# Optimization experiments

Hardware: AMD Instinct MI355X
Metric: run time of the kernel (lower is better)

The kernel has to match this reference:

```python
import jax, jax.numpy as jnp
import numpy as np
import math

B, T, F, H, C = 512, 26, 2048, 1024, 22


def _lstm_cell(x_t, h, c, Wih, Whh, bih, bhh):
    # PyTorch gate order: i, f, g, o. Gates: [B, 4H]
    gates = x_t @ Wih.T + h @ Whh.T + bih + bhh
    i, f, g, o = jnp.split(gates, 4, axis=-1)
    c_new = jax.nn.sigmoid(f) * c + jax.nn.sigmoid(i) * jnp.tanh(g)
    h_new = jax.nn.sigmoid(o) * jnp.tanh(c_new)
    return h_new, c_new


def setup_inputs() -> dict:
    key = jax.random.key(0)
    ks = jax.random.split(key, 13)
    s_enc = 1.0 / math.sqrt(H)
    inp = {
        "x": jax.random.normal(ks[0], (B, T, F), jnp.float32),
        "enc_Wih": jax.random.normal(ks[1], (4 * H, F), jnp.float32) * s_enc,
        "enc_Whh": jax.random.normal(ks[2], (4 * H, H), jnp.float32) * s_enc,
        "enc_bih": jax.random.normal(ks[3], (4 * H,), jnp.float32) * s_enc,
        "enc_bhh": jax.random.normal(ks[4], (4 * H,), jnp.float32) * s_enc,
        "proj_W": jax.random.normal(ks[5], (H, H), jnp.float32) * s_enc,
        "proj_b": jax.random.normal(ks[6], (H,), jnp.float32) * s_enc,
        "dec_Wih": jax.random.normal(ks[7], (4 * H, H + F), jnp.float32) * s_enc,
        "dec_Whh": jax.random.normal(ks[8], (4 * H, H), jnp.float32) * s_enc,
        "dec_bih": jax.random.normal(ks[9], (4 * H,), jnp.float32) * s_enc,
        "dec_bhh": jax.random.normal(ks[10], (4 * H,), jnp.float32) * s_enc,
        "cls_W": jax.random.normal(ks[11], (C, H), jnp.float32) * s_enc,
        "cls_b": jax.random.normal(ks[12], (C,), jnp.float32) * s_enc,
    }
    return inp


def reference(x, enc_Wih, enc_Whh, enc_bih, enc_bhh, proj_W, proj_b,
              dec_Wih, dec_Whh, dec_bih, dec_bhh, cls_W, cls_b):
    # feature_extractor treated as identity (fusion_size == F)
    b, t, _ = x.shape
    h = x.shape[-1]  # noqa (F)

    # ---- Encoder LSTM over time (batch_first) ----
    def enc_step(carry, x_t):
        h_prev, c_prev = carry
        h_new, c_new = _lstm_cell(x_t, h_prev, c_prev, enc_Wih, enc_Whh, enc_bih, enc_bhh)
        return (h_new, c_new), h_new

    h0 = jnp.zeros((b, H), x.dtype)
    c0 = jnp.zeros((b, H), x.dtype)
    xs = jnp.swapaxes(x, 0, 1)  # [T, B, F]
    _, h_ts = jax.lax.scan(enc_step, (h0, c0), xs)  # [T, B, H]
    h_ts = jnp.swapaxes(h_ts, 0, 1)  # [B, T, H]

    proj_h_ts = h_ts @ proj_W.T + proj_b  # [B, T, H]
    inv_sqrt_h = 1.0 / math.sqrt(H)

    # ---- Decoder with per-step attention ----
    def dec_step(carry, x_t):
        dec_h, dec_c = carry
        # attention scores over encoder timesteps
        attn_logits = jnp.einsum('bh,bth->bt', dec_h, proj_h_ts) * inv_sqrt_h
        attn_w = jax.nn.softmax(attn_logits, axis=-1)
        attn = jnp.einsum('bt,bth->bh', attn_w, proj_h_ts)  # [B, H]
        inp_t = jnp.concatenate([x_t, attn], axis=1)  # [B, F+H]
        dec_h, dec_c = _lstm_cell(inp_t, dec_h, dec_c, dec_Wih, dec_Whh, dec_bih, dec_bhh)
        score = dec_h @ cls_W.T + cls_b  # [B, C]
        return (dec_h, dec_c), score

    _, scores = jax.lax.scan(dec_step, (h0, c0), xs)  # [T, B, C]
    return jnp.swapaxes(scores, 0, 1)  # [B, T, C]
```

## Files before the change

### kernel.cpp

```cpp
#include <hip/hip_runtime.h>

#define DB 512
#define DT 26
#define DF 2048
#define DH 1024
#define DG 4096
#define DC 22

typedef unsigned short u16;
typedef u16 u16x8 __attribute__((ext_vector_type(8)));
typedef __bf16 bf16x8 __attribute__((ext_vector_type(8)));
typedef float f32x4 __attribute__((ext_vector_type(4)));

#define MFMA(a, b, c) __builtin_amdgcn_mfma_f32_16x16x32_bf16((a), (b), (c), 0, 0, 0)

__device__ __forceinline__ float sigm(float x) { return 1.f / (1.f + __expf(-x)); }

__device__ __forceinline__ u16 f2b(float v) {
  unsigned u = __float_as_uint(v);
  return (u16)((u + 0x7FFFu + ((u >> 16) & 1u)) >> 16);
}
__device__ __forceinline__ float b2f(u16 h) {
  return __uint_as_float(((unsigned)h) << 16);
}
__device__ __forceinline__ void store_b4(u16* __restrict__ d, size_t o, float4 v) {
  ushort4 s;
  s.x = f2b(v.x); s.y = f2b(v.y); s.z = f2b(v.z); s.w = f2b(v.w);
  *(ushort4*)(d + o) = s;
}

template <int OUTBF>
__global__ __launch_bounds__(256) void gemm_bt(
    const u16* __restrict__ A1, long lda1, int K1,
    const u16* __restrict__ A2, long lda2,
    const u16* __restrict__ B, long ldb, const float* __restrict__ bias,
    void* __restrict__ Cp, long ldc, int M, int N, int K, int W)
{
  constexpr int LR = 72;
  __shared__ __align__(16) u16 sA[64 * LR];
  __shared__ __align__(16) u16 sB[128 * LR];
  const int tid = threadIdx.x, lane = tid & 63;
  const int wid = tid >> 6, wm = wid >> 1, wn = wid & 1;
  const int nbm = M >> 6;
  const int cpx = gridDim.x >> 3;
  const int swz = (blockIdx.x & 7) * cpx + (blockIdx.x >> 3);
  const int grpw = nbm * W;
  const int bn = (swz / grpw) * W + (swz % W);
  const int bm = (swz % grpw) / W;
  const size_t m0 = (size_t)bm << 6, n0 = (size_t)bn << 7;

  const int row = tid >> 3, c8 = tid & 7;
  u16x8 ra[2], rb[4];

  auto loadA = [&](int k0) {
    const u16* p; long lda; int kk;
    if (k0 < K1) { p = A1; lda = lda1; kk = k0; }
    else         { p = A2; lda = lda2; kk = k0 - K1; }
#pragma unroll
    for (int r = 0; r < 2; ++r)
      ra[r] = *(const u16x8*)(p + (m0 + row + r * 32) * (size_t)lda + (size_t)(kk + c8 * 8));
  };
  auto loadB = [&](int k0) {
#pragma unroll
    for (int r = 0; r < 4; ++r)
      rb[r] = *(const u16x8*)(B + (n0 + row + r * 32) * (size_t)ldb + (size_t)(k0 + c8 * 8));
  };
  loadA(0);
  loadB(0);

  f32x4 acc[2][4] = {};
  for (int k0 = 0; k0 < K; k0 += 64) {
    __syncthreads();
#pragma unroll
    for (int r = 0; r < 2; ++r) *(u16x8*)(sA + (row + r * 32) * LR + c8 * 8) = ra[r];
#pragma unroll
    for (int r = 0; r < 4; ++r) *(u16x8*)(sB + (row + r * 32) * LR + c8 * 8) = rb[r];
    __syncthreads();
    if (k0 + 64 < K) { loadA(k0 + 64); loadB(k0 + 64); }
#pragma unroll
    for (int ks = 0; ks < 2; ++ks) {
      const int ko = ks * 32 + (lane >> 4) * 8;
      bf16x8 af[2], bfr[4];
#pragma unroll
      for (int mi = 0; mi < 2; ++mi)
        af[mi] = *(const bf16x8*)(sA + ((wm << 5) + (mi << 4) + (lane & 15)) * LR + ko);
#pragma unroll
      for (int ni = 0; ni < 4; ++ni)
        bfr[ni] = *(const bf16x8*)(sB + ((wn << 6) + (ni << 4) + (lane & 15)) * LR + ko);
#pragma unroll
      for (int mi = 0; mi < 2; ++mi)
#pragma unroll
        for (int ni = 0; ni < 4; ++ni)
          acc[mi][ni] = MFMA(af[mi], bfr[ni], acc[mi][ni]);
    }
  }

#pragma unroll
  for (int mi = 0; mi < 2; ++mi) {
    const int row0 = (wm << 5) + (mi << 4) + ((lane >> 4) << 2);
#pragma unroll
    for (int ni = 0; ni < 4; ++ni) {
      const size_t gn = n0 + (size_t)((wn << 6) + (ni << 4) + (lane & 15));
      const float bv = bias[gn];
#pragma unroll
      for (int r = 0; r < 4; ++r) {
        const size_t gm = m0 + (size_t)(row0 + r);
        const float v = acc[mi][ni][r] + bv;
        if (OUTBF) ((u16*)Cp)[gm * (size_t)ldc + gn] = f2b(v);
        else       ((float*)Cp)[gm * (size_t)ldc + gn] = v;
      }
    }
  }
}

template <int DEC>
__global__ __launch_bounds__(512) void step_gemm(
    const u16* __restrict__ A, long lda, const u16* __restrict__ B, long ldb,
    const u16* __restrict__ xg, long ldxg, float* __restrict__ cst,
    u16* __restrict__ hout, int K, int first, int skipA)
{
  constexpr int LR = 72;
  __shared__ __align__(16) u16 sA[64 * LR];
  __shared__ __align__(16) u16 sB[128 * LR];
  const int tid = threadIdx.x, lane = tid & 63;
  const int wid = tid >> 6, wm = wid >> 1, wn = wid & 1;
  const int cpx = gridDim.x >> 3;
  const int swz = (blockIdx.x & 7) * cpx + (blockIdx.x >> 3);
  const int bn = swz >> 3, bm = swz & 7;
  const size_t m0 = (size_t)bm << 6, n0 = (size_t)bn << 7;

  const int row = tid >> 3, c8 = tid & 7;
  u16x8 ra, rb[2];
  auto loadA = [&](int k0) {
    ra = *(const u16x8*)(A + (m0 + row) * (size_t)lda + (size_t)(k0 + c8 * 8));
  };
  auto loadB = [&](int k0) {
#pragma unroll
    for (int r = 0; r < 2; ++r)
      rb[r] = *(const u16x8*)(B + (n0 + row + r * 64) * (size_t)ldb + (size_t)(k0 + c8 * 8));
  };

  f32x4 acc[4] = {};
  if (!skipA) {
    loadA(0);
    loadB(0);
    for (int k0 = 0; k0 < K; k0 += 64) {
      __syncthreads();
      *(u16x8*)(sA + row * LR + c8 * 8) = ra;
#pragma unroll
      for (int r = 0; r < 2; ++r) *(u16x8*)(sB + (row + r * 64) * LR + c8 * 8) = rb[r];
      __syncthreads();
      if (k0 + 64 < K) { loadA(k0 + 64); loadB(k0 + 64); }
#pragma unroll
      for (int ks = 0; ks < 2; ++ks) {
        const int ko = ks * 32 + (lane >> 4) * 8;
        bf16x8 af, bfr[4];
        af = *(const bf16x8*)(sA + ((wm << 4) + (lane & 15)) * LR + ko);
#pragma unroll
        for (int ni = 0; ni < 4; ++ni)
          bfr[ni] = *(const bf16x8*)(sB + ((wn << 6) + (ni << 4) + (lane & 15)) * LR + ko);
#pragma unroll
        for (int ni = 0; ni < 4; ++ni)
          acc[ni] = MFMA(af, bfr[ni], acc[ni]);
      }
    }
  }

  const int l = lane & 15;
  const int hg = (bn << 5) + (wn << 4) + l;
  const int row0 = (wm << 4) + ((lane >> 4) << 2);
#pragma unroll
  for (int r = 0; r < 4; ++r) {
    const int gm = (int)m0 + row0 + r;
    const u16* xr = xg + (size_t)gm * ldxg + n0 + (wn << 6) + l;
    const float gi = acc[0][r] + b2f(xr[0]);
    const float gf = acc[1][r] + b2f(xr[16]);
    const float gg = acc[2][r] + b2f(xr[32]);
    const float go = acc[3][r] + b2f(xr[48]);
    const size_t ch = ((size_t)gm << 10) + hg;
    const float cp = first ? 0.f : cst[ch];
    const float cn = sigm(gf) * cp + sigm(gi) * tanhf(gg);
    const float hn = sigm(go) * tanhf(cn);
    cst[ch] = cn;
    if (DEC) hout[((size_t)gm << 11) + 1024 + hg] = f2b(hn);
    else     hout[((size_t)gm << 10) + hg] = f2b(hn);
  }
}

__global__ __launch_bounds__(256) void cvt4_kernel(const float* __restrict__ src,
    u16* __restrict__ dst, int n4) {
  for (int i = blockIdx.x * 256 + threadIdx.x; i < n4; i += gridDim.x * 256) {
    float4 v = *(const float4*)(src + (size_t)i * 4);
    store_b4(dst, (size_t)i * 4, v);
  }
}

__global__ __launch_bounds__(256) void pack_perm_kernel(const float* __restrict__ src,
    long ld_src, long scol, int cols4, u16* __restrict__ dst, long ld_dst, long dcol) {
  const int total = DG * cols4;
  for (int i = blockIdx.x * 256 + threadIdx.x; i < total; i += gridDim.x * 256) {
    const int np = i / cols4, c4 = i - np * cols4;
    const int g = (np >> 4) & 3, h = ((np >> 6) << 4) | (np & 15);
    const int n = g * 1024 + h;
    float4 v = *(const float4*)(src + (size_t)n * ld_src + scol + (size_t)c4 * 4);
    store_b4(dst, (size_t)np * ld_dst + dcol + (size_t)c4 * 4, v);
  }
}

__global__ void pack_bias_perm_kernel(const float* __restrict__ a,
    const float* __restrict__ b, float* __restrict__ o) {
  int np = blockIdx.x * 256 + threadIdx.x;
  if (np < DG) {
    const int g = (np >> 4) & 3, h = ((np >> 6) << 4) | (np & 15);
    const int n = g * 1024 + h;
    o[np] = a[n] + b[n];
  }
}

template <int DO_ATTN>
__global__ __launch_bounds__(256) void attn_cls_kernel(
    const u16* __restrict__ projH, const u16* __restrict__ Zr, u16* __restrict__ Zw,
    const float* __restrict__ clsW, const float* __restrict__ clsb,
    float* __restrict__ out, int do_cls, int tprev)
{
  const int b = blockIdx.x, tid = threadIdx.x, lane = tid & 63, wid = tid >> 6;
  __shared__ float redc[DC][4];
  __shared__ float red[DT][4];
  __shared__ float wgt[DT];

  ushort4 hz = *(const ushort4*)(Zr + ((size_t)b << 11) + 1024 + tid * 4);
  float4 hv = make_float4(b2f(hz.x), b2f(hz.y), b2f(hz.z), b2f(hz.w));

  if (do_cls) {
    float acc[DC];
#pragma unroll
    for (int c = 0; c < DC; ++c) {
      const float4 w = *(const float4*)(clsW + ((size_t)c << 10) + tid * 4);
      acc[c] = hv.x * w.x + hv.y * w.y + hv.z * w.z + hv.w * w.w;
    }
#pragma unroll
    for (int c = 0; c < DC; ++c) {
      float v = acc[c];
#pragma unroll
      for (int off = 32; off; off >>= 1) v += __shfl_xor(v, off);
      if (lane == 0) redc[c][wid] = v;
    }
  }

  if (DO_ATTN) {
    float ph[DT][4];
    float p[DT];
#pragma unroll
    for (int t = 0; t < DT; ++t) {
      ushort4 pv = *(const ushort4*)(projH + (((size_t)t * DB + b) << 10) + tid * 4);
      ph[t][0] = b2f(pv.x); ph[t][1] = b2f(pv.y); ph[t][2] = b2f(pv.z); ph[t][3] = b2f(pv.w);
      p[t] = hv.x * ph[t][0] + hv.y * ph[t][1] + hv.z * ph[t][2] + hv.w * ph[t][3];
    }
#pragma unroll
    for (int t = 0; t < DT; ++t) {
#pragma unroll
      for (int off = 32; off; off >>= 1) p[t] += __shfl_xor(p[t], off);
      if (lane == 0) red[t][wid] = p[t];
    }
    __syncthreads();
    if (tid == 0) {
      float lg[DT];
      float mx = -1e30f;
#pragma unroll
      for (int t = 0; t < DT; ++t) {
        lg[t] = (red[t][0] + red[t][1] + red[t][2] + red[t][3]) * 0.03125f;
        mx = fmaxf(mx, lg[t]);
      }
      float s = 0.f;
#pragma unroll
      for (int t = 0; t < DT; ++t) { lg[t] = __expf(lg[t] - mx); s += lg[t]; }
      float inv = 1.f / s;
#pragma unroll
      for (int t = 0; t < DT; ++t) wgt[t] = lg[t] * inv;
    }
    __syncthreads();
    float4 a = make_float4(0, 0, 0, 0);
#pragma unroll
    for (int t = 0; t < DT; ++t) {
      const float w = wgt[t];
      a.x += w * ph[t][0]; a.y += w * ph[t][1]; a.z += w * ph[t][2]; a.w += w * ph[t][3];
    }
    store_b4(Zw, ((size_t)b << 11) + tid * 4, a);
  }

  if (do_cls) {
    __syncthreads();
    if (tid < DC)
      out[((size_t)b * DT + tprev) * DC + tid] =
          redc[tid][0] + redc[tid][1] + redc[tid][2] + redc[tid][3] + clsb[tid];
  }
}

extern "C" void kernel_launch(void* const* d_in, const int* in_sizes, int n_in,
                              void* d_out, int out_size, void* d_ws, size_t ws_size,
                              hipStream_t stream) {
  const float* x    = (const float*)d_in[0];
  const float* eWih = (const float*)d_in[1];
  const float* eWhh = (const float*)d_in[2];
  const float* ebih = (const float*)d_in[3];
  const float* ebhh = (const float*)d_in[4];
  const float* pW   = (const float*)d_in[5];
  const float* pb   = (const float*)d_in[6];
  const float* dWih = (const float*)d_in[7];
  const float* dWhh = (const float*)d_in[8];
  const float* dbih = (const float*)d_in[9];
  const float* dbhh = (const float*)d_in[10];
  const float* clsW = (const float*)d_in[11];
  const float* clsb = (const float*)d_in[12];
  float* out = (float*)d_out;

  char* p = (char*)d_ws;
  auto alloc = [&](size_t bytes) -> void* {
    char* r = p; p += (bytes + 255) & ~(size_t)255; return (void*)r;
  };
  u16* Xb    = (u16*)alloc((size_t)DB * DT * DF * 2);
  u16* eWx   = (u16*)alloc((size_t)DG * 2048 * 2);
  u16* eWh   = (u16*)alloc((size_t)DG * 1024 * 2);
  u16* dWx   = (u16*)alloc((size_t)DG * 2048 * 2);
  u16* dWah  = (u16*)alloc((size_t)DG * 2048 * 2);
  u16* pWb   = (u16*)alloc((size_t)DH * DH * 2);
  u16* Hb    = (u16*)alloc((size_t)DT * DB * DH * 2);
  u16* encXg = (u16*)alloc((size_t)DB * DT * DG * 2);
  u16* decXg = (u16*)alloc((size_t)DB * DT * DG * 2);
  u16* Z0    = (u16*)alloc((size_t)DB * 2048 * 2);
  u16* Z1    = (u16*)alloc((size_t)DB * 2048 * 2);
  float* eCs = (float*)alloc((size_t)DB * DH * 4);
  float* dCs = (float*)alloc((size_t)DB * DH * 4);
  float* ebs = (float*)alloc(DG * 4);
  float* dbs = (float*)alloc(DG * 4);
  u16* projHb = Xb;

  cvt4_kernel<<<2048, 256, 0, stream>>>(x, Xb, (int)((size_t)DB * DT * DF / 4));
  pack_perm_kernel<<<2048, 256, 0, stream>>>(eWih, DF, 0, DF / 4, eWx, 2048, 0);
  pack_perm_kernel<<<2048, 256, 0, stream>>>(eWhh, DH, 0, DH / 4, eWh, 1024, 0);
  pack_perm_kernel<<<2048, 256, 0, stream>>>(dWih, 3072, 0, DF / 4, dWx, 2048, 0);
  pack_perm_kernel<<<2048, 256, 0, stream>>>(dWih, 3072, 2048, DH / 4, dWah, 2048, 0);
  pack_perm_kernel<<<2048, 256, 0, stream>>>(dWhh, DH, 0, DH / 4, dWah, 2048, 1024);
  cvt4_kernel<<<1024, 256, 0, stream>>>(pW, pWb, DH * DH / 4);
  pack_bias_perm_kernel<<<16, 256, 0, stream>>>(ebih, ebhh, ebs);
  pack_bias_perm_kernel<<<16, 256, 0, stream>>>(dbih, dbhh, dbs);
  hipMemsetAsync(Z0, 0, (size_t)DB * 2048 * 2, stream);

  gemm_bt<1><<<6656, 256, 0, stream>>>(
      Xb, DF, DF, Xb, DF, eWx, DF, ebs, encXg, DG, DB * DT, DG, DF, 4);
  gemm_bt<1><<<6656, 256, 0, stream>>>(
      Xb, DF, DF, Xb, DF, dWx, DF, dbs, decXg, DG, DB * DT, DG, DF, 4);

  for (int t = 0; t < DT; ++t) {
    step_gemm<0><<<256, 512, 0, stream>>>(
        (t == 0) ? Hb : (Hb + (size_t)(t - 1) * DB * DH), DH, eWh, DH,
        encXg + (size_t)t * DG, (long)DT * DG, eCs,
        Hb + (size_t)t * DB * DH, 1024, t == 0, t == 0);
  }

  gemm_bt<1><<<1664, 256, 0, stream>>>(
      Hb, DH, DH, Hb, DH, pWb, DH, pb, projHb, DH, DT * DB, DH, DH, 1);

  for (int t = 0; t < DT; ++t) {
    u16* Zc = (t & 1) ? Z1 : Z0;
    u16* Zn = (t & 1) ? Z0 : Z1;
    attn_cls_kernel<1><<<DB, 256, 0, stream>>>(
        projHb, Zc, Zc, clsW, clsb, out, t > 0, t - 1);
    step_gemm<1><<<256, 512, 0, stream>>>(
        Zc, 2048, dWah, 2048, decXg + (size_t)t * DG, (long)DT * DG, dCs, Zn,
        (t == 0) ? 1024 : 2048, t == 0, 0);
  }
  attn_cls_kernel<0><<<DB, 256, 0, stream>>>(
      projHb, Z0, Z0, clsW, clsb, out, 1, DT - 1);
}
```

Before: 2.140 ms.

## Enlarge GEMM tile to 128x128 and load tiles directly into LDS

```diff
diff --git a/kernel.cpp b/kernel.cpp
--- a/kernel.cpp
+++ b/kernel.cpp
@@ -36,59 +36,50 @@
     const u16* __restrict__ B, long ldb, const float* __restrict__ bias,
     void* __restrict__ Cp, long ldc, int M, int N, int K, int W)
 {
-  constexpr int LR = 72;
-  __shared__ __align__(16) u16 sA[64 * LR];
-  __shared__ __align__(16) u16 sB[128 * LR];
-  const int tid = threadIdx.x, lane = tid & 63;
-  const int wid = tid >> 6, wm = wid >> 1, wn = wid & 1;
-  const int nbm = M >> 6;
+  __shared__ __align__(16) u16 sA[128 * 64];
+  __shared__ __align__(16) u16 sB[128 * 64];
+  const int tid = threadIdx.x, lane = tid & 63, wid = tid >> 6;
+  const int wm = wid >> 1, wn = wid & 1;
+  const int l15 = lane & 15, l4 = lane >> 4;
+  const int nbm = M >> 7;
   const int cpx = gridDim.x >> 3;
   const int swz = (blockIdx.x & 7) * cpx + (blockIdx.x >> 3);
   const int grpw = nbm * W;
   const int bn = (swz / grpw) * W + (swz % W);
   const int bm = (swz % grpw) / W;
-  const size_t m0 = (size_t)bm << 6, n0 = (size_t)bn << 7;
-
-  const int row = tid >> 3, c8 = tid & 7;
-  u16x8 ra[2], rb[4];
-
-  auto loadA = [&](int k0) {
-    const u16* p; long lda; int kk;
-    if (k0 < K1) { p = A1; lda = lda1; kk = k0; }
-    else         { p = A2; lda = lda2; kk = k0 - K1; }
-#pragma unroll
-    for (int r = 0; r < 2; ++r)
-      ra[r] = *(const u16x8*)(p + (m0 + row + r * 32) * (size_t)lda + (size_t)(kk + c8 * 8));
-  };
-  auto loadB = [&](int k0) {
-#pragma unroll
-    for (int r = 0; r < 4; ++r)
-      rb[r] = *(const u16x8*)(B + (n0 + row + r * 32) * (size_t)ldb + (size_t)(k0 + c8 * 8));
-  };
-  loadA(0);
-  loadB(0);
-
-  f32x4 acc[2][4] = {};
+  const size_t m0 = (size_t)bm << 7, n0 = (size_t)bn << 7;
+
+  f32x4 acc[4][4] = {};
   for (int k0 = 0; k0 < K; k0 += 64) {
-    __syncthreads();
-#pragma unroll
-    for (int r = 0; r < 2; ++r) *(u16x8*)(sA + (row + r * 32) * LR + c8 * 8) = ra[r];
-#pragma unroll
-    for (int r = 0; r < 4; ++r) *(u16x8*)(sB + (row + r * 32) * LR + c8 * 8) = rb[r];
-    __syncthreads();
-    if (k0 + 64 < K) { loadA(k0 + 64); loadB(k0 + 64); }
+    const u16* pA; long lda; int kk;
+    if (k0 < K1) { pA = A1; lda = lda1; kk = k0; }
+    else         { pA = A2; lda = lda2; kk = k0 - K1; }
+    __syncthreads();
+#pragma unroll
+    for (int g = 0; g < 4; ++g) {
+      const int cb = (wid * 4 + g) * 64;
+      const int chunk = cb + lane;
+      const int row = chunk >> 3, c8 = chunk & 7;
+      __builtin_amdgcn_global_load_lds(
+          (const __attribute__((address_space(1))) void*)(pA + (m0 + row) * (size_t)lda + kk + c8 * 8),
+          (__attribute__((address_space(3))) void*)((char*)sA + cb * 16), 16, 0, 0);
+      __builtin_amdgcn_global_load_lds(
+          (const __attribute__((address_space(1))) void*)(B + (n0 + row) * (size_t)ldb + k0 + c8 * 8),
+          (__attribute__((address_space(3))) void*)((char*)sB + cb * 16), 16, 0, 0);
+    }
+    __syncthreads();
 #pragma unroll
     for (int ks = 0; ks < 2; ++ks) {
-      const int ko = ks * 32 + (lane >> 4) * 8;
-      bf16x8 af[2], bfr[4];
-#pragma unroll
-      for (int mi = 0; mi < 2; ++mi)
-        af[mi] = *(const bf16x8*)(sA + ((wm << 5) + (mi << 4) + (lane & 15)) * LR + ko);
+      const int ko = ks * 32 + l4 * 8;
+      bf16x8 af[4], bfr[4];
+#pragma unroll
+      for (int mi = 0; mi < 4; ++mi)
+        af[mi] = *(const bf16x8*)(sA + ((wm << 6) + (mi << 4) + l15) * 64 + ko);
 #pragma unroll
       for (int ni = 0; ni < 4; ++ni)
-        bfr[ni] = *(const bf16x8*)(sB + ((wn << 6) + (ni << 4) + (lane & 15)) * LR + ko);
-#pragma unroll
-      for (int mi = 0; mi < 2; ++mi)
+        bfr[ni] = *(const bf16x8*)(sB + ((wn << 6) + (ni << 4) + l15) * 64 + ko);
+#pragma unroll
+      for (int mi = 0; mi < 4; ++mi)
 #pragma unroll
         for (int ni = 0; ni < 4; ++ni)
           acc[mi][ni] = MFMA(af[mi], bfr[ni], acc[mi][ni]);
@@ -96,11 +87,11 @@
   }
 
 #pragma unroll
-  for (int mi = 0; mi < 2; ++mi) {
-    const int row0 = (wm << 5) + (mi << 4) + ((lane >> 4) << 2);
+  for (int mi = 0; mi < 4; ++mi) {
+    const int row0 = (wm << 6) + (mi << 4) + (l4 << 2);
 #pragma unroll
     for (int ni = 0; ni < 4; ++ni) {
-      const size_t gn = n0 + (size_t)((wn << 6) + (ni << 4) + (lane & 15));
+      const size_t gn = n0 + (size_t)((wn << 6) + (ni << 4) + l15);
       const float bv = bias[gn];
 #pragma unroll
       for (int r = 0; r < 4; ++r) {
@@ -346,9 +337,9 @@
   pack_bias_perm_kernel<<<16, 256, 0, stream>>>(dbih, dbhh, dbs);
   hipMemsetAsync(Z0, 0, (size_t)DB * 2048 * 2, stream);
 
-  gemm_bt<1><<<6656, 256, 0, stream>>>(
+  gemm_bt<1><<<3328, 256, 0, stream>>>(
       Xb, DF, DF, Xb, DF, eWx, DF, ebs, encXg, DG, DB * DT, DG, DF, 4);
-  gemm_bt<1><<<6656, 256, 0, stream>>>(
+  gemm_bt<1><<<3328, 256, 0, stream>>>(
       Xb, DF, DF, Xb, DF, dWx, DF, dbs, decXg, DG, DB * DT, DG, DF, 4);
 
   for (int t = 0; t < DT; ++t) {
@@ -358,7 +349,7 @@
         Hb + (size_t)t * DB * DH, 1024, t == 0, t == 0);
   }
 
-  gemm_bt<1><<<1664, 256, 0, stream>>>(
+  gemm_bt<1><<<832, 256, 0, stream>>>(
       Hb, DH, DH, Hb, DH, pWb, DH, pb, projHb, DH, DT * DB, DH, DH, 1);
 
   for (int t = 0; t < DT; ++t) {
```

New measurement: 2.238 ms. 4.6% more time.
